# Kernel tuning notes

Measured on AMD Instinct MI355X. Metric: run time of the kernel, lower is better.

The kernel has to match this reference:

```python
import jax, jax.numpy as jnp
import numpy as np

N_NODES = 32
N_EDGES = N_NODES * (N_NODES - 1)  # 992
BATCH = 16
SEQ = 8
BS = BATCH * SEQ  # 128 frames
D = 256  # node_latent_dim == edge_latent_dim
ITERS = 3


def gru_cell(x, h, Wih, Whh, bih, bhh):
    # torch GRUCell: gates ordered (r, z, n)
    gi = x @ Wih.T + bih
    gh = h @ Whh.T + bhh
    ir, iz, inn = jnp.split(gi, 3, axis=-1)
    hr, hz, hn = jnp.split(gh, 3, axis=-1)
    r = jax.nn.sigmoid(ir + hr)
    z = jax.nn.sigmoid(iz + hz)
    n = jnp.tanh(inn + r * hn)
    return (1.0 - z) * n + z * h


def setup_inputs() -> dict:
    key = jax.random.key(0)
    ks = jax.random.split(key, 16)
    s = 0.05
    inp = {
        'node_latents': jax.random.normal(ks[0], (BS * N_NODES, D), jnp.float32),
        'edge_latents': jax.random.normal(ks[1], (BS * N_EDGES, D), jnp.float32),
        'node_Wih': jax.random.normal(ks[2], (3 * D, D), jnp.float32) * s,
        'node_Whh': jax.random.normal(ks[3], (3 * D, D), jnp.float32) * s,
        'node_bih': jax.random.normal(ks[4], (3 * D,), jnp.float32) * s,
        'node_bhh': jax.random.normal(ks[5], (3 * D,), jnp.float32) * s,
        'edge_Wih': jax.random.normal(ks[6], (3 * D, D), jnp.float32) * s,
        'edge_Whh': jax.random.normal(ks[7], (3 * D, D), jnp.float32) * s,
        'edge_bih': jax.random.normal(ks[8], (3 * D,), jnp.float32) * s,
        'edge_bhh': jax.random.normal(ks[9], (3 * D,), jnp.float32) * s,
        'w_node_pool': jax.random.normal(ks[10], (2 * D,), jnp.float32) * s,
        'w_edge_pool_sub': jax.random.normal(ks[11], (2 * D,), jnp.float32) * s,
        'w_edge_pool_obj': jax.random.normal(ks[12], (2 * D,), jnp.float32) * s,
    }
    # all ordered (subject, object) pairs with subject != object, same for every frame
    pairs = np.array([(i, j) for i in range(N_NODES) for j in range(N_NODES) if i != j], dtype=np.int32)  # [E,2]
    e2n = np.concatenate([np.arange(N_EDGES, dtype=np.int32)[:, None], pairs], axis=1)  # [E,3]
    inp['edge_idx_to_node_idxs'] = jnp.asarray(np.broadcast_to(e2n, (BS, N_EDGES, 3)).copy())
    return inp


def reference(node_latents, edge_latents, node_Wih, node_Whh, node_bih, node_bhh,
              edge_Wih, edge_Whh, edge_bih, edge_bhh,
              w_node_pool, w_edge_pool_sub, w_edge_pool_obj, edge_idx_to_node_idxs):
    sub = edge_idx_to_node_idxs[..., 1].astype(jnp.int32)  # [BS,E]
    obj = edge_idx_to_node_idxs[..., 2].astype(jnp.int32)
    bidx = jnp.arange(BS, dtype=jnp.int32)[:, None]
    sub_flat = (bidx * N_NODES + sub).reshape(-1)  # [BS*E]
    obj_flat = (bidx * N_NODES + obj).reshape(-1)

    # initial GRU call with zero hidden state (torch GRUCell default)
    node_hidden = gru_cell(node_latents, jnp.zeros_like(node_latents), node_Wih, node_Whh, node_bih, node_bhh)
    edge_hidden = gru_cell(edge_latents, jnp.zeros_like(edge_latents), edge_Wih, edge_Whh, edge_bih, edge_bhh)

    for _ in range(ITERS):
        nh = node_hidden.reshape(BS, N_NODES, D)
        eh = edge_hidden.reshape(BS, N_EDGES, D)
        ns = jnp.take_along_axis(nh, sub[:, :, None], axis=1)  # [BS,E,D] subject node feats
        no = jnp.take_along_axis(nh, obj[:, :, None], axis=1)  # [BS,E,D]
        cat_s = jnp.concatenate([ns, eh], axis=-1)  # [BS,E,2D]
        cat_o = jnp.concatenate([no, eh], axis=-1)
        g_node = jax.nn.sigmoid(cat_s @ w_node_pool)[..., None]        # [BS,E,1]
        g_sub = jax.nn.sigmoid(cat_s @ w_edge_pool_sub)[..., None]
        g_obj = jax.nn.sigmoid(cat_o @ w_edge_pool_obj)[..., None]
        # node message: gated edge features scattered to subject and object nodes
        # (equivalent to the dense 0/1 incidence matmul since subject != object per edge)
        msg_e = (g_node * eh).reshape(-1, D)  # [BS*E,D]
        node_msg = (jax.ops.segment_sum(msg_e, sub_flat, num_segments=BS * N_NODES)
                    + jax.ops.segment_sum(msg_e, obj_flat, num_segments=BS * N_NODES))  # [BS*N,D]
        edge_msg = (g_sub * ns + g_obj * no).reshape(-1, D)  # [BS*E,D]
        node_hidden = gru_cell(node_msg, node_hidden, node_Wih, node_Whh, node_bih, node_bhh)
        edge_hidden = gru_cell(edge_msg, edge_hidden, edge_Wih, edge_Whh, edge_bih, edge_bhh)

    return (node_hidden.reshape(BS, N_NODES, D), edge_hidden.reshape(BS, N_EDGES, D))
```

## Files before the change

kernel.cpp:

```cpp
#include <hip/hip_runtime.h>


#define D_DIM 256
#define NNODE 32
#define NEDGE 992
#define EDGE_ROWS (128 * NEDGE)
#define NODE_ROWS (128 * NNODE)
#define BM 64
#define EGRID (EDGE_ROWS / BM)
#define NGRID (NODE_ROWS / BM)
#define GI_OFF 32768
#define GI_STR 776

typedef _Float16 half8 __attribute__((ext_vector_type(8)));
typedef __attribute__((ext_vector_type(4))) float f32x4;

__device__ __forceinline__ float sigf(float x) { return 1.0f / (1.0f + __expf(-x)); }
__device__ __forceinline__ float tanh_fast(float x) { return 2.0f / (1.0f + __expf(-2.0f * x)) - 1.0f; }
__device__ __forceinline__ float dot4(float4 a, float4 b) { return a.x*b.x + a.y*b.y + a.z*b.z + a.w*b.w; }

__global__ __launch_bounds__(64) void pack_w(const float* __restrict__ Wih,
                                             const float* __restrict__ Whh,
                                             _Float16* __restrict__ ph) {
  const int ct = blockIdx.x;
  const int ks = blockIdx.y;
  const int l = threadIdx.x;
  const int col = ct * 16 + (l & 15);
  const int kb = ks * 32 + (l >> 4) * 8;
  const float* src = (kb < 256) ? (Wih + col * 256 + kb) : (Whh + col * 256 + (kb - 256));
  half8 v;
  #pragma unroll
  for (int j = 0; j < 8; ++j) v[j] = (_Float16)src[j];
  *(half8*)(ph + ((ct * 16 + ks) * 64 + l) * 8) = v;
}

__global__ __launch_bounds__(1024, 4) void gru_init(
    const float* __restrict__ xe, const float* __restrict__ xn,
    float* __restrict__ he, float* __restrict__ hn,
    const _Float16* __restrict__ wpe, const _Float16* __restrict__ wpn,
    const float* __restrict__ ebih, const float* __restrict__ ebhh,
    const float* __restrict__ nbih, const float* __restrict__ nbhh) {
  __shared__ __align__(16) unsigned char lds[32768];
  const bool edge = blockIdx.x < EGRID;
  const int bx = edge ? blockIdx.x : (blockIdx.x - EGRID);
  const float* xsrc = edge ? xe : xn;
  float* h = edge ? he : hn;
  const _Float16* wp = edge ? wpe : wpn;
  const float* bih = edge ? ebih : nbih;
  const float* bhh = edge ? ebhh : nbhh;

  const int t = threadIdx.x;
  const int rb = bx * BM;
  const int srow = t >> 4;
  const int skc = t & 15;
  const int w = t >> 6;
  const int l = t & 63;
  const int lq = l >> 4;
  const int lr = l & 15;
  const int swm = (lr & 7) << 4;
  const int swz = (srow & 7) << 4;
  const int rowg = rb + srow;

  #pragma unroll
  for (int c = 0; c < 2; ++c) {
    half8 hx;
    #pragma unroll
    for (int pq = 0; pq < 2; ++pq) {
      const float4 a = *(const float4*)(xsrc + rowg * D_DIM + c * 128 + skc * 8 + pq * 4);
      hx[pq * 4 + 0] = (_Float16)a.x; hx[pq * 4 + 1] = (_Float16)a.y;
      hx[pq * 4 + 2] = (_Float16)a.z; hx[pq * 4 + 3] = (_Float16)a.w;
    }
    *(half8*)(&lds[(srow * 512 + c * 256 + skc * 16) ^ swz]) = hx;
  }
  __syncthreads();

  const f32x4 zz = {0.f, 0.f, 0.f, 0.f};
  f32x4 acc_r[4] = {zz, zz, zz, zz};
  f32x4 acc_z[4] = {zz, zz, zz, zz};
  f32x4 acc_nx[4] = {zz, zz, zz, zz};

  #pragma unroll
  for (int ksg = 0; ksg < 8; ++ksg) {
    half8 ah[4];
    #pragma unroll
    for (int rf = 0; rf < 4; ++rf)
      ah[rf] = *(const half8*)(&lds[((rf * 16 + lr) * 512 + ksg * 64 + lq * 16) ^ swm]);
    const half8 br_ = *(const half8*)(wp + (((0 * 16 + w) * 16 + ksg) * 64 + l) * 8);
    const half8 bz_ = *(const half8*)(wp + (((1 * 16 + w) * 16 + ksg) * 64 + l) * 8);
    const half8 bn_ = *(const half8*)(wp + (((2 * 16 + w) * 16 + ksg) * 64 + l) * 8);
    #pragma unroll
    for (int rf = 0; rf < 4; ++rf)
      acc_r[rf] = __builtin_amdgcn_mfma_f32_16x16x32_f16(ah[rf], br_, acc_r[rf], 0, 0, 0);
    #pragma unroll
    for (int rf = 0; rf < 4; ++rf)
      acc_z[rf] = __builtin_amdgcn_mfma_f32_16x16x32_f16(ah[rf], bz_, acc_z[rf], 0, 0, 0);
    #pragma unroll
    for (int rf = 0; rf < 4; ++rf)
      acc_nx[rf] = __builtin_amdgcn_mfma_f32_16x16x32_f16(ah[rf], bn_, acc_nx[rf], 0, 0, 0);
  }

  const int col = w * 16 + lr;
  const float br = bih[col] + bhh[col];
  const float bz = bih[256 + col] + bhh[256 + col];
  const float bnx = bih[512 + col];
  const float bnh = bhh[512 + col];
  #pragma unroll
  for (int rf = 0; rf < 4; ++rf) {
    #pragma unroll
    for (int q = 0; q < 4; ++q) {
      const int rowl = rf * 16 + lq * 4 + q;
      const float r = sigf(acc_r[rf][q] + br);
      const float z = sigf(acc_z[rf][q] + bz);
      const float n = tanh_fast(acc_nx[rf][q] + bnx + r * bnh);
      h[(rb + rowl) * D_DIM + col] = (1.0f - z) * n;
    }
  }
}

__global__ __launch_bounds__(1024, 4) void gru_nw(
    const float* __restrict__ nh, const _Float16* __restrict__ wp,
    _Float16* __restrict__ nw,
    const float* __restrict__ wnp, const float* __restrict__ wes,
    const float* __restrict__ weo,
    float* __restrict__ dA, float* __restrict__ dS, float* __restrict__ dO) {
  __shared__ __align__(16) unsigned char lds[32768];
  const int t = threadIdx.x;
  const int rb = blockIdx.x * BM;
  const int srow = t >> 4;
  const int skc = t & 15;
  const int w = t >> 6;
  const int l = t & 63;
  const int lq = l >> 4;
  const int lr = l & 15;
  const int swm = (lr & 7) << 4;
  const int swz = (srow & 7) << 4;
  const int rowg = rb + srow;

  float4 xa[4];
  #pragma unroll
  for (int i = 0; i < 4; ++i)
    xa[i] = *(const float4*)(nh + rowg * D_DIM + (i >> 1) * 128 + skc * 8 + (i & 1) * 4);
  #pragma unroll
  for (int c = 0; c < 2; ++c) {
    half8 hx;
    const float* f0 = (const float*)&xa[c * 2];
    #pragma unroll
    for (int j = 0; j < 8; ++j) hx[j] = (_Float16)f0[j];
    *(half8*)(&lds[(srow * 512 + c * 256 + skc * 16) ^ swz]) = hx;
  }
  float p1 = 0.f, p2 = 0.f, p3 = 0.f;
  #pragma unroll
  for (int i = 0; i < 4; ++i) {
    const int k0 = (i >> 1) * 128 + skc * 8 + (i & 1) * 4;
    p1 += dot4(xa[i], *(const float4*)(wnp + k0));
    p2 += dot4(xa[i], *(const float4*)(wes + k0));
    p3 += dot4(xa[i], *(const float4*)(weo + k0));
  }
  #pragma unroll
  for (int mm = 1; mm < 16; mm <<= 1) {
    p1 += __shfl_xor(p1, mm, 16);
    p2 += __shfl_xor(p2, mm, 16);
    p3 += __shfl_xor(p3, mm, 16);
  }
  if (skc == 0) { dA[rowg] = p1; dS[rowg] = p2; dO[rowg] = p3; }
  __syncthreads();

  const f32x4 zz = {0.f, 0.f, 0.f, 0.f};
  f32x4 acc_r[4] = {zz, zz, zz, zz};
  f32x4 acc_z[4] = {zz, zz, zz, zz};
  f32x4 acc_nx[4] = {zz, zz, zz, zz};

  #pragma unroll
  for (int ksg = 0; ksg < 8; ++ksg) {
    half8 ah[4];
    #pragma unroll
    for (int rf = 0; rf < 4; ++rf)
      ah[rf] = *(const half8*)(&lds[((rf * 16 + lr) * 512 + ksg * 64 + lq * 16) ^ swm]);
    const half8 br_ = *(const half8*)(wp + (((0 * 16 + w) * 16 + ksg) * 64 + l) * 8);
    const half8 bz_ = *(const half8*)(wp + (((1 * 16 + w) * 16 + ksg) * 64 + l) * 8);
    const half8 bn_ = *(const half8*)(wp + (((2 * 16 + w) * 16 + ksg) * 64 + l) * 8);
    #pragma unroll
    for (int rf = 0; rf < 4; ++rf)
      acc_r[rf] = __builtin_amdgcn_mfma_f32_16x16x32_f16(ah[rf], br_, acc_r[rf], 0, 0, 0);
    #pragma unroll
    for (int rf = 0; rf < 4; ++rf)
      acc_z[rf] = __builtin_amdgcn_mfma_f32_16x16x32_f16(ah[rf], bz_, acc_z[rf], 0, 0, 0);
    #pragma unroll
    for (int rf = 0; rf < 4; ++rf)
      acc_nx[rf] = __builtin_amdgcn_mfma_f32_16x16x32_f16(ah[rf], bn_, acc_nx[rf], 0, 0, 0);
  }

  const int col = w * 16 + lr;
  #pragma unroll
  for (int rf = 0; rf < 4; ++rf) {
    #pragma unroll
    for (int q = 0; q < 4; ++q) {
      const int rowl = rf * 16 + lq * 4 + q;
      _Float16* np = nw + (rb + rowl) * 768 + col;
      np[0]   = (_Float16)acc_r[rf][q];
      np[256] = (_Float16)acc_z[rf][q];
      np[512] = (_Float16)acc_nx[rf][q];
    }
  }
}

__global__ __launch_bounds__(1024, 4) void gru_iter(
    float* __restrict__ eh, float* __restrict__ nh,
    const float* __restrict__ nmsg,
    const _Float16* __restrict__ wpe, const _Float16* __restrict__ wpn,
    const float* __restrict__ ebih, const float* __restrict__ ebhh,
    const float* __restrict__ nbih, const float* __restrict__ nbhh,
    const float* __restrict__ wesb, const float* __restrict__ weob,
    const float* __restrict__ dotS, const float* __restrict__ dotO,
    const _Float16* __restrict__ nw) {
  __shared__ __align__(16) unsigned char lds[32768 + BM * GI_STR * 2];

  const int t = threadIdx.x;
  const int srow = t >> 4;
  const int skc = t & 15;
  const int w = t >> 6;
  const int l = t & 63;
  const int lq = l >> 4;
  const int lr = l & 15;
  const int swm = (lr & 7) << 4;
  const int swz = (srow & 7) << 4;

  const f32x4 zz = {0.f, 0.f, 0.f, 0.f};
  f32x4 acc_r[4] = {zz, zz, zz, zz};
  f32x4 acc_z[4] = {zz, zz, zz, zz};
  f32x4 acc_nx[4] = {zz, zz, zz, zz};
  f32x4 acc_nh[4] = {zz, zz, zz, zz};

  if (blockIdx.x < EGRID) {
    const int rb = blockIdx.x * BM;
    const int rowg = rb + srow;
    const int b = rowg / NEDGE;
    const int e = rowg - b * NEDGE;
    const int si = e / 31;
    const int m = e - si * 31;
    const int ob = (m < si) ? m : (m + 1);

    float4 pre[4];
    #pragma unroll
    for (int i = 0; i < 4; ++i)
      pre[i] = *(const float4*)(eh + rowg * D_DIM + (i >> 1) * 128 + skc * 8 + (i & 1) * 4);
    #pragma unroll
    for (int c = 0; c < 2; ++c) {
      half8 hh8;
      const float* f1 = (const float*)&pre[c * 2];
      #pragma unroll
      for (int j = 0; j < 8; ++j) hh8[j] = (_Float16)f1[j];
      *(half8*)(&lds[(srow * 512 + c * 256 + skc * 16) ^ swz]) = hh8;
    }
    float pS = 0.f, pO = 0.f;
    #pragma unroll
    for (int i = 0; i < 4; ++i) {
      const int k0 = (i >> 1) * 128 + skc * 8 + (i & 1) * 4;
      pS += dot4(pre[i], *(const float4*)(wesb + k0));
      pO += dot4(pre[i], *(const float4*)(weob + k0));
    }
    #pragma unroll
    for (int mm = 1; mm < 16; mm <<= 1) {
      pS += __shfl_xor(pS, mm, 16);
      pO += __shfl_xor(pO, mm, 16);
    }
    const float gs = sigf(dotS[b * NNODE + si] + pS);
    const float go = sigf(dotO[b * NNODE + ob] + pO);
    const _Float16 gsh = (_Float16)gs, goh = (_Float16)go;
    const _Float16* ns = nw + (b * NNODE + si) * 768;
    const _Float16* no_ = nw + (b * NNODE + ob) * 768;
    _Float16* giw = (_Float16*)(lds + GI_OFF) + srow * GI_STR;
    #pragma unroll
    for (int j = 0; j < 6; ++j) {
      const int c0 = skc * 8 + j * 128;
      const half8 a = *(const half8*)(ns + c0);
      const half8 bb = *(const half8*)(no_ + c0);
      half8 g;
      #pragma unroll
      for (int k = 0; k < 8; ++k) g[k] = gsh * a[k] + goh * bb[k];
      *(half8*)(giw + c0) = g;
    }
    __syncthreads();

    #pragma unroll
    for (int ksg = 0; ksg < 8; ++ksg) {
      half8 ah[4];
      #pragma unroll
      for (int rf = 0; rf < 4; ++rf)
        ah[rf] = *(const half8*)(&lds[((rf * 16 + lr) * 512 + ksg * 64 + lq * 16) ^ swm]);
      const int kk = 8 + ksg;
      const half8 br_ = *(const half8*)(wpe + (((0 * 16 + w) * 16 + kk) * 64 + l) * 8);
      const half8 bz_ = *(const half8*)(wpe + (((1 * 16 + w) * 16 + kk) * 64 + l) * 8);
      const half8 bn_ = *(const half8*)(wpe + (((2 * 16 + w) * 16 + kk) * 64 + l) * 8);
      #pragma unroll
      for (int rf = 0; rf < 4; ++rf)
        acc_r[rf] = __builtin_amdgcn_mfma_f32_16x16x32_f16(ah[rf], br_, acc_r[rf], 0, 0, 0);
      #pragma unroll
      for (int rf = 0; rf < 4; ++rf)
        acc_z[rf] = __builtin_amdgcn_mfma_f32_16x16x32_f16(ah[rf], bz_, acc_z[rf], 0, 0, 0);
      #pragma unroll
      for (int rf = 0; rf < 4; ++rf)
        acc_nh[rf] = __builtin_amdgcn_mfma_f32_16x16x32_f16(ah[rf], bn_, acc_nh[rf], 0, 0, 0);
    }

    const int col = w * 16 + lr;
    const float br = ebih[col] + ebhh[col];
    const float bz = ebih[256 + col] + ebhh[256 + col];
    const float bnx = ebih[512 + col];
    const float bnh = ebhh[512 + col];
    const _Float16* gir = (const _Float16*)(lds + GI_OFF);
    #pragma unroll
    for (int rf = 0; rf < 4; ++rf) {
      #pragma unroll
      for (int q = 0; q < 4; ++q) {
        const int rowl = rf * 16 + lq * 4 + q;
        const _Float16* gp = gir + rowl * GI_STR + col;
        const float r = sigf(acc_r[rf][q] + (float)gp[0] + br);
        const float z = sigf(acc_z[rf][q] + (float)gp[256] + bz);
        const float n = tanh_fast((float)gp[512] + bnx + r * (acc_nh[rf][q] + bnh));
        const float hv = eh[(rb + rowl) * D_DIM + col];
        eh[(rb + rowl) * D_DIM + col] = (1.0f - z) * n + z * hv;
      }
    }
  } else {
    const int rb = (blockIdx.x - EGRID) * BM;
    const int rowg = rb + srow;

    {
      float4 pre[4];
      #pragma unroll
      for (int i = 0; i < 4; ++i)
        pre[i] = *(const float4*)(nh + rowg * D_DIM + (i >> 1) * 128 + skc * 8 + (i & 1) * 4);
      #pragma unroll
      for (int c = 0; c < 2; ++c) {
        half8 hh8;
        const float* f1 = (const float*)&pre[c * 2];
        #pragma unroll
        for (int j = 0; j < 8; ++j) hh8[j] = (_Float16)f1[j];
        *(half8*)(&lds[(srow * 1024 + 512 + c * 256 + skc * 16) ^ swz]) = hh8;
      }
    }
    __syncthreads();

    #pragma unroll
    for (int ksg = 0; ksg < 8; ++ksg) {
      half8 ah[4];
      #pragma unroll
      for (int rf = 0; rf < 4; ++rf)
        ah[rf] = *(const half8*)(&lds[((rf * 16 + lr) * 1024 + 512 + ksg * 64 + lq * 16) ^ swm]);
      const int kk = 8 + ksg;
      const half8 br_ = *(const half8*)(wpn + (((0 * 16 + w) * 16 + kk) * 64 + l) * 8);
      const half8 bz_ = *(const half8*)(wpn + (((1 * 16 + w) * 16 + kk) * 64 + l) * 8);
      const half8 bn_ = *(const half8*)(wpn + (((2 * 16 + w) * 16 + kk) * 64 + l) * 8);
      #pragma unroll
      for (int rf = 0; rf < 4; ++rf)
        acc_r[rf] = __builtin_amdgcn_mfma_f32_16x16x32_f16(ah[rf], br_, acc_r[rf], 0, 0, 0);
      #pragma unroll
      for (int rf = 0; rf < 4; ++rf)
        acc_z[rf] = __builtin_amdgcn_mfma_f32_16x16x32_f16(ah[rf], bz_, acc_z[rf], 0, 0, 0);
      #pragma unroll
      for (int rf = 0; rf < 4; ++rf)
        acc_nh[rf] = __builtin_amdgcn_mfma_f32_16x16x32_f16(ah[rf], bn_, acc_nh[rf], 0, 0, 0);
    }

    #pragma unroll
    for (int c = 0; c < 2; ++c) {
      half8 hx;
      #pragma unroll
      for (int pq = 0; pq < 2; ++pq) {
        const float4 a = *(const float4*)(nmsg + rowg * D_DIM + c * 128 + skc * 8 + pq * 4);
        hx[pq * 4 + 0] = (_Float16)a.x; hx[pq * 4 + 1] = (_Float16)a.y;
        hx[pq * 4 + 2] = (_Float16)a.z; hx[pq * 4 + 3] = (_Float16)a.w;
      }
      *(half8*)(&lds[(srow * 1024 + 0 + c * 256 + skc * 16) ^ swz]) = hx;
    }
    __syncthreads();
    #pragma unroll
    for (int ksg = 0; ksg < 8; ++ksg) {
      half8 ah[4];
      #pragma unroll
      for (int rf = 0; rf < 4; ++rf)
        ah[rf] = *(const half8*)(&lds[((rf * 16 + lr) * 1024 + 0 + ksg * 64 + lq * 16) ^ swm]);
      const half8 br_ = *(const half8*)(wpn + (((0 * 16 + w) * 16 + ksg) * 64 + l) * 8);
      const half8 bz_ = *(const half8*)(wpn + (((1 * 16 + w) * 16 + ksg) * 64 + l) * 8);
      const half8 bn_ = *(const half8*)(wpn + (((2 * 16 + w) * 16 + ksg) * 64 + l) * 8);
      #pragma unroll
      for (int rf = 0; rf < 4; ++rf)
        acc_r[rf] = __builtin_amdgcn_mfma_f32_16x16x32_f16(ah[rf], br_, acc_r[rf], 0, 0, 0);
      #pragma unroll
      for (int rf = 0; rf < 4; ++rf)
        acc_z[rf] = __builtin_amdgcn_mfma_f32_16x16x32_f16(ah[rf], bz_, acc_z[rf], 0, 0, 0);
      #pragma unroll
      for (int rf = 0; rf < 4; ++rf)
        acc_nx[rf] = __builtin_amdgcn_mfma_f32_16x16x32_f16(ah[rf], bn_, acc_nx[rf], 0, 0, 0);
    }

    const int col = w * 16 + lr;
    const float br = nbih[col] + nbhh[col];
    const float bz = nbih[256 + col] + nbhh[256 + col];
    const float bnx = nbih[512 + col];
    const float bnh = nbhh[512 + col];
    #pragma unroll
    for (int rf = 0; rf < 4; ++rf) {
      #pragma unroll
      for (int q = 0; q < 4; ++q) {
        const int rowl = rf * 16 + lq * 4 + q;
        const float r = sigf(acc_r[rf][q] + br);
        const float z = sigf(acc_z[rf][q] + bz);
        const float n = tanh_fast(acc_nx[rf][q] + bnx + r * (acc_nh[rf][q] + bnh));
        const float hv = nh[(rb + rowl) * D_DIM + col];
        nh[(rb + rowl) * D_DIM + col] = (1.0f - z) * n + z * hv;
      }
    }
  }
}

__global__ __launch_bounds__(256) void node_msg_kernel(
    const float* __restrict__ eh, const float* __restrict__ wnp,
    const float* __restrict__ dotA, float* __restrict__ nmsg) {
  __shared__ float sh[3][256];
  const int nr = blockIdx.x;
  const int b = nr >> 5;
  const int n = nr & 31;
  const int wv = threadIdx.x >> 6;
  const int l = threadIdx.x & 63;
  const int base = b * NEDGE;
  const float4 w1b = ((const float4*)(wnp + 256))[l];

  float4 acc = {0.f, 0.f, 0.f, 0.f};
  for (int k = wv; k < 62; k += 4) {
    int e, sub;
    if (k < 31) {
      e = base + n * 31 + k;
      sub = n;
    } else {
      int i = k - 31;
      const int ip = (i < n) ? i : (i + 1);
      e = base + ip * 31 + ((n < ip) ? n : (n - 1));
      sub = ip;
    }
    const float4 ev = ((const float4*)(eh + e * D_DIM))[l];
    float p = dot4(ev, w1b);
    #pragma unroll
    for (int mm = 32; mm > 0; mm >>= 1) p += __shfl_xor(p, mm, 64);
    const float gN = sigf(dotA[b * NNODE + sub] + p);
    acc.x += gN * ev.x; acc.y += gN * ev.y; acc.z += gN * ev.z; acc.w += gN * ev.w;
  }
  if (wv > 0) *(float4*)(&sh[wv - 1][l * 4]) = acc;
  __syncthreads();
  if (wv == 0) {
    #pragma unroll
    for (int v = 0; v < 3; ++v) {
      const float4 o = *(const float4*)(&sh[v][l * 4]);
      acc.x += o.x; acc.y += o.y; acc.z += o.z; acc.w += o.w;
    }
    *(float4*)(nmsg + nr * D_DIM + l * 4) = acc;
  }
}

extern "C" void kernel_launch(void* const* d_in, const int* in_sizes, int n_in,
                              void* d_out, int out_size, void* d_ws, size_t ws_size,
                              hipStream_t stream) {
  const float* node_latents = (const float*)d_in[0];
  const float* edge_latents = (const float*)d_in[1];
  const float* node_Wih = (const float*)d_in[2];
  const float* node_Whh = (const float*)d_in[3];
  const float* node_bih = (const float*)d_in[4];
  const float* node_bhh = (const float*)d_in[5];
  const float* edge_Wih = (const float*)d_in[6];
  const float* edge_Whh = (const float*)d_in[7];
  const float* edge_bih = (const float*)d_in[8];
  const float* edge_bhh = (const float*)d_in[9];
  const float* w_node_pool = (const float*)d_in[10];
  const float* w_edge_sub = (const float*)d_in[11];
  const float* w_edge_obj = (const float*)d_in[12];

  float* nh = (float*)d_out;
  float* eh = (float*)d_out + NODE_ROWS * D_DIM;

  const int WPLANE = 48 * 16 * 64 * 8;
  _Float16* ph_n = (_Float16*)d_ws;
  _Float16* ph_e = ph_n + WPLANE;
  _Float16* NW = ph_e + WPLANE;
  float* fw = (float*)(NW + NODE_ROWS * 768);
  float* dotA = fw; fw += NODE_ROWS;
  float* dotS = fw; fw += NODE_ROWS;
  float* dotO = fw; fw += NODE_ROWS;
  float* node_msg = fw; fw += NODE_ROWS * D_DIM;

  dim3 pg(48, 16);
  pack_w<<<pg, 64, 0, stream>>>(node_Wih, node_Whh, ph_n);
  pack_w<<<pg, 64, 0, stream>>>(edge_Wih, edge_Whh, ph_e);

  gru_init<<<EGRID + NGRID, 1024, 0, stream>>>(
      edge_latents, node_latents, eh, nh, ph_e, ph_n,
      edge_bih, edge_bhh, node_bih, node_bhh);

  for (int it = 0; it < 3; ++it) {
    gru_nw<<<NGRID, 1024, 0, stream>>>(
        nh, ph_e, NW, w_node_pool, w_edge_sub, w_edge_obj, dotA, dotS, dotO);
    node_msg_kernel<<<NODE_ROWS, 256, 0, stream>>>(eh, w_node_pool, dotA, node_msg);
    gru_iter<<<EGRID + NGRID, 1024, 0, stream>>>(
        eh, nh, node_msg, ph_e, ph_n,
        edge_bih, edge_bhh, node_bih, node_bhh,
        w_edge_sub + 256, w_edge_obj + 256, dotS, dotO, NW);
  }
}
```

Baseline: 715.6 us.

## Store intermediate edge hidden state as fp16 with LDS-staged coalesced writes

Edge hidden state between iterations is now kept in an fp16 workspace instead of fp32 in the output buffer. gru_init and the non-final gru_iter stage results through LDS and write them as coalesced 16-byte chunks, while only the last iteration writes fp32 to the output. The old hidden value is read back from LDS instead of global memory, and node_msg_kernel reads fp16. This roughly halves edge-state memory traffic, the dominant cost, at the price of fp16 rounding of the recurrent state and extra syncthreads.

```diff
diff --git a/kernel.cpp b/kernel.cpp
--- a/kernel.cpp
+++ b/kernel.cpp
@@ -13,6 +13,7 @@
 #define GI_STR 776
 
 typedef _Float16 half8 __attribute__((ext_vector_type(8)));
+typedef _Float16 half4v __attribute__((ext_vector_type(4)));
 typedef __attribute__((ext_vector_type(4))) float f32x4;
 
 __device__ __forceinline__ float sigf(float x) { return 1.0f / (1.0f + __expf(-x)); }
@@ -36,7 +37,7 @@
 
 __global__ __launch_bounds__(1024, 4) void gru_init(
     const float* __restrict__ xe, const float* __restrict__ xn,
-    float* __restrict__ he, float* __restrict__ hn,
+    _Float16* __restrict__ eh16, float* __restrict__ hn,
     const _Float16* __restrict__ wpe, const _Float16* __restrict__ wpn,
     const float* __restrict__ ebih, const float* __restrict__ ebhh,
     const float* __restrict__ nbih, const float* __restrict__ nbhh) {
@@ -44,7 +45,6 @@
   const bool edge = blockIdx.x < EGRID;
   const int bx = edge ? blockIdx.x : (blockIdx.x - EGRID);
   const float* xsrc = edge ? xe : xn;
-  float* h = edge ? he : hn;
   const _Float16* wp = edge ? wpe : wpn;
   const float* bih = edge ? ebih : nbih;
   const float* bhh = edge ? ebhh : nbhh;
@@ -104,15 +104,48 @@
   const float bz = bih[256 + col] + bhh[256 + col];
   const float bnx = bih[512 + col];
   const float bnh = bhh[512 + col];
-  #pragma unroll
-  for (int rf = 0; rf < 4; ++rf) {
-    #pragma unroll
-    for (int q = 0; q < 4; ++q) {
-      const int rowl = rf * 16 + lq * 4 + q;
-      const float r = sigf(acc_r[rf][q] + br);
-      const float z = sigf(acc_z[rf][q] + bz);
-      const float n = tanh_fast(acc_nx[rf][q] + bnx + r * bnh);
-      h[(rb + rowl) * D_DIM + col] = (1.0f - z) * n;
+
+  if (edge) {
+    _Float16 sv[16];
+    #pragma unroll
+    for (int rf = 0; rf < 4; ++rf) {
+      #pragma unroll
+      for (int q = 0; q < 4; ++q) {
+        const float r = sigf(acc_r[rf][q] + br);
+        const float z = sigf(acc_z[rf][q] + bz);
+        const float n = tanh_fast(acc_nx[rf][q] + bnx + r * bnh);
+        sv[rf * 4 + q] = (_Float16)((1.0f - z) * n);
+      }
+    }
+    __syncthreads();
+    #pragma unroll
+    for (int rf = 0; rf < 4; ++rf) {
+      #pragma unroll
+      for (int q = 0; q < 4; ++q) {
+        const int rowl = rf * 16 + lq * 4 + q;
+        *(_Float16*)(&lds[(rowl * 512 + col * 2) ^ ((rowl & 7) << 4)]) = sv[rf * 4 + q];
+      }
+    }
+    __syncthreads();
+    #pragma unroll
+    for (int p = 0; p < 2; ++p) {
+      const int c = t + p * 1024;
+      const int row = c >> 5;
+      const int kc = c & 31;
+      *(uint4*)(eh16 + (rb + row) * 256 + kc * 8) =
+          *(const uint4*)(&lds[(row * 512 + kc * 16) ^ ((row & 7) << 4)]);
+    }
+  } else {
+    #pragma unroll
+    for (int rf = 0; rf < 4; ++rf) {
+      #pragma unroll
+      for (int q = 0; q < 4; ++q) {
+        const int rowl = rf * 16 + lq * 4 + q;
+        const float r = sigf(acc_r[rf][q] + br);
+        const float z = sigf(acc_z[rf][q] + bz);
+        const float n = tanh_fast(acc_nx[rf][q] + bnx + r * bnh);
+        hn[(rb + rowl) * D_DIM + col] = (1.0f - z) * n;
+      }
     }
   }
 }
@@ -204,9 +237,10 @@
   }
 }
 
+template <bool LAST>
 __global__ __launch_bounds__(1024, 4) void gru_iter(
-    float* __restrict__ eh, float* __restrict__ nh,
-    const float* __restrict__ nmsg,
+    _Float16* __restrict__ eh16, float* __restrict__ ehf,
+    float* __restrict__ nh, const float* __restrict__ nmsg,
     const _Float16* __restrict__ wpe, const _Float16* __restrict__ wpn,
     const float* __restrict__ ebih, const float* __restrict__ ebhh,
     const float* __restrict__ nbih, const float* __restrict__ nbhh,
@@ -240,24 +274,21 @@
     const int m = e - si * 31;
     const int ob = (m < si) ? m : (m + 1);
 
-    float4 pre[4];
-    #pragma unroll
-    for (int i = 0; i < 4; ++i)
-      pre[i] = *(const float4*)(eh + rowg * D_DIM + (i >> 1) * 128 + skc * 8 + (i & 1) * 4);
-    #pragma unroll
-    for (int c = 0; c < 2; ++c) {
-      half8 hh8;
-      const float* f1 = (const float*)&pre[c * 2];
-      #pragma unroll
-      for (int j = 0; j < 8; ++j) hh8[j] = (_Float16)f1[j];
-      *(half8*)(&lds[(srow * 512 + c * 256 + skc * 16) ^ swz]) = hh8;
-    }
+    const uint4 v0 = *(const uint4*)(eh16 + rowg * 256 + skc * 8);
+    const uint4 v1 = *(const uint4*)(eh16 + rowg * 256 + 128 + skc * 8);
+    *(uint4*)(&lds[(srow * 512 + skc * 16) ^ swz]) = v0;
+    *(uint4*)(&lds[(srow * 512 + 256 + skc * 16) ^ swz]) = v1;
     float pS = 0.f, pO = 0.f;
-    #pragma unroll
-    for (int i = 0; i < 4; ++i) {
-      const int k0 = (i >> 1) * 128 + skc * 8 + (i & 1) * 4;
-      pS += dot4(pre[i], *(const float4*)(wesb + k0));
-      pO += dot4(pre[i], *(const float4*)(weob + k0));
+    {
+      const _Float16* f0 = (const _Float16*)&v0;
+      const _Float16* f1 = (const _Float16*)&v1;
+      #pragma unroll
+      for (int j = 0; j < 8; ++j) {
+        const float a = (float)f0[j];
+        const float bb = (float)f1[j];
+        pS += a * wesb[skc * 8 + j] + bb * wesb[128 + skc * 8 + j];
+        pO += a * weob[skc * 8 + j] + bb * weob[128 + skc * 8 + j];
+      }
     }
     #pragma unroll
     for (int mm = 1; mm < 16; mm <<= 1) {
@@ -309,6 +340,7 @@
     const float bnx = ebih[512 + col];
     const float bnh = ebhh[512 + col];
     const _Float16* gir = (const _Float16*)(lds + GI_OFF);
+    _Float16 sv[16];
     #pragma unroll
     for (int rf = 0; rf < 4; ++rf) {
       #pragma unroll
@@ -318,8 +350,34 @@
         const float r = sigf(acc_r[rf][q] + (float)gp[0] + br);
         const float z = sigf(acc_z[rf][q] + (float)gp[256] + bz);
         const float n = tanh_fast((float)gp[512] + bnx + r * (acc_nh[rf][q] + bnh));
-        const float hv = eh[(rb + rowl) * D_DIM + col];
-        eh[(rb + rowl) * D_DIM + col] = (1.0f - z) * n + z * hv;
+        const float hv =
+            (float)*(const _Float16*)(&lds[(rowl * 512 + col * 2) ^ ((rowl & 7) << 4)]);
+        const float out = (1.0f - z) * n + z * hv;
+        if constexpr (LAST) {
+          ehf[(rb + rowl) * D_DIM + col] = out;
+        } else {
+          sv[rf * 4 + q] = (_Float16)out;
+        }
+      }
+    }
+    if constexpr (!LAST) {
+      __syncthreads();
+      #pragma unroll
+      for (int rf = 0; rf < 4; ++rf) {
+        #pragma unroll
+        for (int q = 0; q < 4; ++q) {
+          const int rowl = rf * 16 + lq * 4 + q;
+          *(_Float16*)(&lds[(rowl * 512 + col * 2) ^ ((rowl & 7) << 4)]) = sv[rf * 4 + q];
+        }
+      }
+      __syncthreads();
+      #pragma unroll
+      for (int p = 0; p < 2; ++p) {
+        const int c = t + p * 1024;
+        const int row = c >> 5;
+        const int kc = c & 31;
+        *(uint4*)(eh16 + (rb + row) * 256 + kc * 8) =
+            *(const uint4*)(&lds[(row * 512 + kc * 16) ^ ((row & 7) << 4)]);
       }
     }
   } else {
@@ -416,7 +474,7 @@
 }
 
 __global__ __launch_bounds__(256) void node_msg_kernel(
-    const float* __restrict__ eh, const float* __restrict__ wnp,
+    const _Float16* __restrict__ eh16, const float* __restrict__ wnp,
     const float* __restrict__ dotA, float* __restrict__ nmsg) {
   __shared__ float sh[3][256];
   const int nr = blockIdx.x;
@@ -439,7 +497,10 @@
       e = base + ip * 31 + ((n < ip) ? n : (n - 1));
       sub = ip;
     }
-    const float4 ev = ((const float4*)(eh + e * D_DIM))[l];
+    const half4v hv4 = ((const half4v*)(eh16 + e * 256))[l];
+    float4 ev;
+    ev.x = (float)hv4[0]; ev.y = (float)hv4[1];
+    ev.z = (float)hv4[2]; ev.w = (float)hv4[3];
     float p = dot4(ev, w1b);
     #pragma unroll
     for (int mm = 32; mm > 0; mm >>= 1) p += __shfl_xor(p, mm, 64);
@@ -482,7 +543,8 @@
   _Float16* ph_n = (_Float16*)d_ws;
   _Float16* ph_e = ph_n + WPLANE;
   _Float16* NW = ph_e + WPLANE;
-  float* fw = (float*)(NW + NODE_ROWS * 768);
+  _Float16* eh16 = NW + NODE_ROWS * 768;
+  float* fw = (float*)(eh16 + (size_t)EDGE_ROWS * D_DIM);
   float* dotA = fw; fw += NODE_ROWS;
   float* dotS = fw; fw += NODE_ROWS;
   float* dotO = fw; fw += NODE_ROWS;
@@ -493,16 +555,22 @@
   pack_w<<<pg, 64, 0, stream>>>(edge_Wih, edge_Whh, ph_e);
 
   gru_init<<<EGRID + NGRID, 1024, 0, stream>>>(
-      edge_latents, node_latents, eh, nh, ph_e, ph_n,
+      edge_latents, node_latents, eh16, nh, ph_e, ph_n,
       edge_bih, edge_bhh, node_bih, node_bhh);
 
   for (int it = 0; it < 3; ++it) {
     gru_nw<<<NGRID, 1024, 0, stream>>>(
         nh, ph_e, NW, w_node_pool, w_edge_sub, w_edge_obj, dotA, dotS, dotO);
-    node_msg_kernel<<<NODE_ROWS, 256, 0, stream>>>(eh, w_node_pool, dotA, node_msg);
-    gru_iter<<<EGRID + NGRID, 1024, 0, stream>>>(
-        eh, nh, node_msg, ph_e, ph_n,
-        edge_bih, edge_bhh, node_bih, node_bhh,
-        w_edge_sub + 256, w_edge_obj + 256, dotS, dotO, NW);
+    node_msg_kernel<<<NODE_ROWS, 256, 0, stream>>>(eh16, w_node_pool, dotA, node_msg);
+    if (it < 2)
+      gru_iter<false><<<EGRID + NGRID, 1024, 0, stream>>>(
+          eh16, eh, nh, node_msg, ph_e, ph_n,
+          edge_bih, edge_bhh, node_bih, node_bhh,
+          w_edge_sub + 256, w_edge_obj + 256, dotS, dotO, NW);
+    else
+      gru_iter<true><<<EGRID + NGRID, 1024, 0, stream>>>(
+          eh16, eh, nh, node_msg, ph_e, ph_n,
+          edge_bih, edge_bhh, node_bih, node_bhh,
+          w_edge_sub + 256, w_edge_obj + 256, dotS, dotO, NW);
   }
 }
```

After: 656.4 us (median of 3 runs). -8.3%, faster.
